# Optimization experiments

Hardware: AMD Instinct MI355X
Metric: run time of the kernel (lower is better)

Reference implementation:

```python
import jax, jax.numpy as jnp
import numpy as np

E, R, CIN, COUT = 8, 8, 256, 256
B, H, W = 16, 64, 64
DN = ('NCHW', 'OIHW', 'NCHW')


def setup_inputs() -> dict:
    key = jax.random.key(0)
    k1, k2, k3, k4 = jax.random.split(key, 4)
    x = jax.random.normal(k1, (B, CIN, H, W), jnp.float32)
    probs = jax.nn.softmax(jax.random.normal(k2, (E,), jnp.float32))
    # in conv: rank filters over in_channels, kernel (1,3); out conv: kernel (3,1)
    weight_in = jax.random.normal(k3, (E, R, CIN, 1, 3), jnp.float32) * 0.02
    weight_out = jax.random.normal(k4, (E, COUT, R, 3, 1), jnp.float32) * 0.02
    return {"x": x, "probs": probs, "weight_in": weight_in, "weight_out": weight_out}


def _expert_conv(x, w_in, w_out):
    # in conv: stride (1,1), padding (0,1) -> [B,R,H,W]
    h = jax.lax.conv_general_dilated(x, w_in, window_strides=(1, 1),
                                     padding=[(0, 0), (1, 1)], dimension_numbers=DN)
    # out conv: stride (1,1), padding (1,0) -> [B,COUT,H,W]
    return jax.lax.conv_general_dilated(h, w_out, window_strides=(1, 1),
                                        padding=[(1, 1), (0, 0)], dimension_numbers=DN)


def reference(x, probs, weight_in, weight_out):
    # vmap over experts replaces the Python loop; outs: [E,B,COUT,H,W]
    outs = jax.vmap(lambda wi, wo: _expert_conv(x, wi, wo))(weight_in, weight_out)
    # probability-weighted sum over experts (stack + sum in the original)
    return jnp.einsum('e,ebchw->bchw', probs, outs)
```

## Files before the change

kernel.cpp:

```cpp
#include <hip/hip_runtime.h>
#include <hip/hip_bf16.h>


typedef __bf16 bf16x8 __attribute__((ext_vector_type(8)));
typedef __bf16 bf16x4 __attribute__((ext_vector_type(4)));
typedef float  f32x4  __attribute__((ext_vector_type(4)));

#define CIN_  256
#define COUT_ 256
#define M1    64
#define K1    768
#define K2    192
#define CS    264
#define HS2   264

static __device__ __forceinline__ unsigned short f2bf(float f) {
    union { float f; unsigned u; } v; v.f = f;
    unsigned r = v.u + 0x7FFFu + ((v.u >> 16) & 1u);
    return (unsigned short)(r >> 16);
}

__global__ void prep_weights(const float* __restrict__ probs,
                             const float* __restrict__ w_in,
                             const float* __restrict__ w_out,
                             unsigned short* __restrict__ W1,
                             unsigned short* __restrict__ W2) {
    int idx = blockIdx.x * blockDim.x + threadIdx.x;
    if (idx < M1 * K1) {
        int er = idx / K1, rem = idx % K1;
        int kx = rem / CIN_, c = rem % CIN_;
        int e = er >> 3;
        W1[idx] = f2bf(probs[e] * w_in[(er * CIN_ + c) * 3 + kx]);
    } else {
        int i2 = idx - M1 * K1;
        int o = i2 / K2, rem = i2 % K2;
        int ky = rem / M1, er = rem % M1;
        int e = er >> 3, r = er & 7;
        W2[i2] = f2bf(w_out[((e * COUT_ + o) * 8 + r) * 3 + ky]);
    }
}

__global__ __launch_bounds__(256, 2)
void fused_kernel(const float* __restrict__ x,
                  const unsigned short* __restrict__ W1,
                  const unsigned short* __restrict__ W2,
                  float* __restrict__ out) {
    __shared__ unsigned short xs[66 * CS];
    __shared__ unsigned short hs[64 * HS2];
    const int bid  = blockIdx.x;
    const int b    = bid >> 5;
    const int y0   = (bid & 31) << 1;
    const int tid  = threadIdx.x;
    const int lane = tid & 63;
    const int wave = tid >> 6;
    const int g    = lane >> 4;
    const int lr   = lane & 15;

    bf16x8 w1f[3][8];
    {
        const unsigned short* w1p = W1 + (wave * 16 + lr) * K1 + g * 8;
        #pragma unroll
        for (int kx = 0; kx < 3; ++kx)
            #pragma unroll
            for (int cc = 0; cc < 8; ++cc)
                w1f[kx][cc] = *(const bf16x8*)(w1p + kx * CIN_ + cc * 32);
    }

    if (tid < 66) {
        int row = (tid < 33) ? 0 : 65;
        int col = (tid - (tid < 33 ? 0 : 33)) * 8;
        bf16x4 z4 = {};
        *(bf16x4*)&xs[row * CS + col] = z4;
        *(bf16x4*)&xs[row * CS + col + 4] = z4;
    }

    const int crow = tid >> 4;
    const int n4   = (tid & 15) << 2;
    const int swzt = (tid & 7) << 3;

    for (int yy = 0; yy < 4; ++yy) {
        const int y = y0 - 1 + yy;
        const bool yok = ((unsigned)y < 64u);
        __syncthreads();
        const float* xbase = x + ((b * CIN_ + crow) * 64 + (yok ? y : 0)) * 64 + n4;
        unsigned short* wr = &xs[(n4 + 1) * CS];
        #pragma unroll
        for (int r = 0; r < 4; ++r) {
            float4 ld[4];
            if (yok) {
                #pragma unroll
                for (int q = 0; q < 4; ++q)
                    ld[q] = *(const float4*)(xbase + (r * 4 + q) * 16 * 4096);
            } else {
                #pragma unroll
                for (int q = 0; q < 4; ++q) ld[q] = make_float4(0.f, 0.f, 0.f, 0.f);
            }
            #pragma unroll
            for (int q = 0; q < 4; ++q) {
                int cx = ((r * 4 + q) * 16 + crow) ^ swzt;
                wr[0 * CS + cx] = f2bf(ld[q].x);
                wr[1 * CS + cx] = f2bf(ld[q].y);
                wr[2 * CS + cx] = f2bf(ld[q].z);
                wr[3 * CS + cx] = f2bf(ld[q].w);
            }
        }
        __syncthreads();

        f32x4 acc[4];
        #pragma unroll
        for (int i = 0; i < 4; ++i) acc[i] = (f32x4){0.f, 0.f, 0.f, 0.f};
        #pragma unroll
        for (int kx = 0; kx < 3; ++kx) {
            int ns0 = lr + kx;
            int sz0 = (((ns0 - 1) >> 2) & 7) << 3;
            int ns1 = ns0 + 16, sz1 = (((ns1 - 1) >> 2) & 7) << 3;
            int ns2 = ns0 + 32, sz2 = (((ns2 - 1) >> 2) & 7) << 3;
            int ns3 = ns0 + 48, sz3 = (((ns3 - 1) >> 2) & 7) << 3;
            const unsigned short* r0  = &xs[ns0 * CS];
            const unsigned short* r1  = &xs[ns1 * CS];
            const unsigned short* r2p = &xs[ns2 * CS];
            const unsigned short* r3  = &xs[ns3 * CS];
            #pragma unroll
            for (int cc = 0; cc < 8; ++cc) {
                int co = cc * 32 + g * 8;
                acc[0] = __builtin_amdgcn_mfma_f32_16x16x32_bf16(
                    w1f[kx][cc], *(const bf16x8*)&r0[co ^ sz0], acc[0], 0, 0, 0);
                acc[1] = __builtin_amdgcn_mfma_f32_16x16x32_bf16(
                    w1f[kx][cc], *(const bf16x8*)&r1[co ^ sz1], acc[1], 0, 0, 0);
                acc[2] = __builtin_amdgcn_mfma_f32_16x16x32_bf16(
                    w1f[kx][cc], *(const bf16x8*)&r2p[co ^ sz2], acc[2], 0, 0, 0);
                acc[3] = __builtin_amdgcn_mfma_f32_16x16x32_bf16(
                    w1f[kx][cc], *(const bf16x8*)&r3[co ^ sz3], acc[3], 0, 0, 0);
            }
        }
        #pragma unroll
        for (int nt = 0; nt < 4; ++nt) {
            int n = nt * 16 + lr;
            bf16x4 pk;
            #pragma unroll
            for (int r2 = 0; r2 < 4; ++r2) pk[r2] = (__bf16)acc[nt][r2];
            int col = (yy * 64 + wave * 16 + g * 4) ^ ((n & 7) << 3);
            *(bf16x4*)&hs[n * HS2 + col] = pk;
        }
    }
    __syncthreads();

    bf16x8 w2f[4][6];
    #pragma unroll
    for (int ot = 0; ot < 4; ++ot)
        #pragma unroll
        for (int kc = 0; kc < 6; ++kc)
            w2f[ot][kc] = *(const bf16x8*)(W2 + ((wave * 4 + ot) * 16 + lr) * K2 +
                                           kc * 32 + g * 8);

    #pragma unroll
    for (int ry = 0; ry < 2; ++ry) {
        f32x4 acc2[4][4];
        #pragma unroll
        for (int ot = 0; ot < 4; ++ot)
            #pragma unroll
            for (int nt = 0; nt < 4; ++nt) acc2[ot][nt] = (f32x4){0.f, 0.f, 0.f, 0.f};

        #pragma unroll
        for (int kc = 0; kc < 6; ++kc) {
            bf16x8 bfrag[4];
            #pragma unroll
            for (int nt = 0; nt < 4; ++nt) {
                int n = nt * 16 + lr;
                int col = (ry * 64 + kc * 32 + g * 8) ^ ((n & 7) << 3);
                bfrag[nt] = *(const bf16x8*)&hs[n * HS2 + col];
            }
            #pragma unroll
            for (int ot = 0; ot < 4; ++ot)
                #pragma unroll
                for (int nt = 0; nt < 4; ++nt)
                    acc2[ot][nt] = __builtin_amdgcn_mfma_f32_16x16x32_bf16(
                        w2f[ot][kc], bfrag[nt], acc2[ot][nt], 0, 0, 0);
        }

        const int yo = y0 + ry;
        #pragma unroll
        for (int ot = 0; ot < 4; ++ot) {
            #pragma unroll
            for (int r2 = 0; r2 < 4; ++r2) {
                int o = (wave * 4 + ot) * 16 + g * 4 + r2;
                float* orow = out + ((b * COUT_ + o) * 64 + yo) * 64;
                #pragma unroll
                for (int nt = 0; nt < 4; ++nt)
                    orow[nt * 16 + lr] = acc2[ot][nt][r2];
            }
        }
    }
}

extern "C" void kernel_launch(void* const* d_in, const int* in_sizes, int n_in,
                              void* d_out, int out_size, void* d_ws, size_t ws_size,
                              hipStream_t stream) {
    const float* x     = (const float*)d_in[0];
    const float* probs = (const float*)d_in[1];
    const float* w_in  = (const float*)d_in[2];
    const float* w_out = (const float*)d_in[3];
    float* out = (float*)d_out;

    unsigned short* W1 = (unsigned short*)d_ws;
    unsigned short* W2 = W1 + M1 * K1;

    prep_weights<<<384, 256, 0, stream>>>(probs, w_in, w_out, W1, W2);
    fused_kernel<<<16 * 32, 256, 0, stream>>>(x, W1, W2, out);
}
```

Before: 49.25 us.

## Prefetch next input row into registers and pack bf16x4 LDS stores with new swizzle

```diff
diff --git a/kernel.cpp b/kernel.cpp
--- a/kernel.cpp
+++ b/kernel.cpp
@@ -11,13 +11,17 @@
 #define M1    64
 #define K1    768
 #define K2    192
-#define CS    264
-#define HS2   264
+#define CS    256
+#define HS    256
 
 static __device__ __forceinline__ unsigned short f2bf(float f) {
     union { float f; unsigned u; } v; v.f = f;
     unsigned r = v.u + 0x7FFFu + ((v.u >> 16) & 1u);
     return (unsigned short)(r >> 16);
+}
+
+static __device__ __forceinline__ int qsw(int r) {
+    return ((r ^ (r >> 3)) & 7) << 3;
 }
 
 __global__ void prep_weights(const float* __restrict__ probs,
@@ -46,7 +50,7 @@
                   const unsigned short* __restrict__ W2,
                   float* __restrict__ out) {
     __shared__ unsigned short xs[66 * CS];
-    __shared__ unsigned short hs[64 * HS2];
+    __shared__ unsigned short hs[64 * HS];
     const int bid  = blockIdx.x;
     const int b    = bid >> 5;
     const int y0   = (bid & 31) << 1;
@@ -66,92 +70,110 @@
                 w1f[kx][cc] = *(const bf16x8*)(w1p + kx * CIN_ + cc * 32);
     }
 
-    if (tid < 66) {
-        int row = (tid < 33) ? 0 : 65;
-        int col = (tid - (tid < 33 ? 0 : 33)) * 8;
-        bf16x4 z4 = {};
-        *(bf16x4*)&xs[row * CS + col] = z4;
-        *(bf16x4*)&xs[row * CS + col + 4] = z4;
-    }
-
-    const int crow = tid >> 4;
-    const int n4   = (tid & 15) << 2;
-    const int swzt = (tid & 7) << 3;
-
+    if (tid < 64) {
+        int row = (tid < 32) ? 0 : 65;
+        int col = (tid & 31) * 8;
+        bf16x8 z = {};
+        *(bf16x8*)&xs[row * CS + col] = z;
+    }
+
+    const int c0b = (tid >> 4) << 2;
+    const int n4  = (tid & 15) << 2;
+
+    f32x4 ld[4][4];
+
+    {
+        const int y = y0 - 1;
+        if (y >= 0) {
+            const float* xb = x + ((b * CIN_ + c0b) * 64 + y) * 64 + n4;
+            #pragma unroll
+            for (int it = 0; it < 4; ++it)
+                #pragma unroll
+                for (int i = 0; i < 4; ++i)
+                    ld[it][i] = *(const f32x4*)(xb + (it * 64 + i) * 4096);
+        } else {
+            #pragma unroll
+            for (int it = 0; it < 4; ++it)
+                #pragma unroll
+                for (int i = 0; i < 4; ++i)
+                    ld[it][i] = (f32x4){0.f, 0.f, 0.f, 0.f};
+        }
+    }
+
+    bf16x8 w2f[4][6];
+
+    #pragma unroll
     for (int yy = 0; yy < 4; ++yy) {
-        const int y = y0 - 1 + yy;
-        const bool yok = ((unsigned)y < 64u);
         __syncthreads();
-        const float* xbase = x + ((b * CIN_ + crow) * 64 + (yok ? y : 0)) * 64 + n4;
-        unsigned short* wr = &xs[(n4 + 1) * CS];
-        #pragma unroll
-        for (int r = 0; r < 4; ++r) {
-            float4 ld[4];
-            if (yok) {
-                #pragma unroll
-                for (int q = 0; q < 4; ++q)
-                    ld[q] = *(const float4*)(xbase + (r * 4 + q) * 16 * 4096);
+        #pragma unroll
+        for (int it = 0; it < 4; ++it) {
+            #pragma unroll
+            for (int j = 0; j < 4; ++j) {
+                int row = n4 + 1 + j;
+                int col = (it * 64 + c0b) ^ qsw(n4 + j);
+                bf16x4 pk;
+                #pragma unroll
+                for (int i = 0; i < 4; ++i) pk[i] = (__bf16)ld[it][i][j];
+                *(bf16x4*)&xs[row * CS + col] = pk;
+            }
+        }
+        __syncthreads();
+
+        if (yy < 3) {
+            const int y = y0 + yy;
+            if (y < 64) {
+                const float* xb = x + ((b * CIN_ + c0b) * 64 + y) * 64 + n4;
+                #pragma unroll
+                for (int it = 0; it < 4; ++it)
+                    #pragma unroll
+                    for (int i = 0; i < 4; ++i)
+                        ld[it][i] = *(const f32x4*)(xb + (it * 64 + i) * 4096);
             } else {
                 #pragma unroll
-                for (int q = 0; q < 4; ++q) ld[q] = make_float4(0.f, 0.f, 0.f, 0.f);
-            }
-            #pragma unroll
-            for (int q = 0; q < 4; ++q) {
-                int cx = ((r * 4 + q) * 16 + crow) ^ swzt;
-                wr[0 * CS + cx] = f2bf(ld[q].x);
-                wr[1 * CS + cx] = f2bf(ld[q].y);
-                wr[2 * CS + cx] = f2bf(ld[q].z);
-                wr[3 * CS + cx] = f2bf(ld[q].w);
-            }
-        }
-        __syncthreads();
+                for (int it = 0; it < 4; ++it)
+                    #pragma unroll
+                    for (int i = 0; i < 4; ++i)
+                        ld[it][i] = (f32x4){0.f, 0.f, 0.f, 0.f};
+            }
+        } else {
+            #pragma unroll
+            for (int ot = 0; ot < 4; ++ot)
+                #pragma unroll
+                for (int kc = 0; kc < 6; ++kc)
+                    w2f[ot][kc] = *(const bf16x8*)(W2 +
+                        ((wave * 4 + ot) * 16 + lr) * K2 + kc * 32 + g * 8);
+        }
 
         f32x4 acc[4];
         #pragma unroll
         for (int i = 0; i < 4; ++i) acc[i] = (f32x4){0.f, 0.f, 0.f, 0.f};
+
         #pragma unroll
         for (int kx = 0; kx < 3; ++kx) {
-            int ns0 = lr + kx;
-            int sz0 = (((ns0 - 1) >> 2) & 7) << 3;
-            int ns1 = ns0 + 16, sz1 = (((ns1 - 1) >> 2) & 7) << 3;
-            int ns2 = ns0 + 32, sz2 = (((ns2 - 1) >> 2) & 7) << 3;
-            int ns3 = ns0 + 48, sz3 = (((ns3 - 1) >> 2) & 7) << 3;
-            const unsigned short* r0  = &xs[ns0 * CS];
-            const unsigned short* r1  = &xs[ns1 * CS];
-            const unsigned short* r2p = &xs[ns2 * CS];
-            const unsigned short* r3  = &xs[ns3 * CS];
             #pragma unroll
             for (int cc = 0; cc < 8; ++cc) {
-                int co = cc * 32 + g * 8;
-                acc[0] = __builtin_amdgcn_mfma_f32_16x16x32_bf16(
-                    w1f[kx][cc], *(const bf16x8*)&r0[co ^ sz0], acc[0], 0, 0, 0);
-                acc[1] = __builtin_amdgcn_mfma_f32_16x16x32_bf16(
-                    w1f[kx][cc], *(const bf16x8*)&r1[co ^ sz1], acc[1], 0, 0, 0);
-                acc[2] = __builtin_amdgcn_mfma_f32_16x16x32_bf16(
-                    w1f[kx][cc], *(const bf16x8*)&r2p[co ^ sz2], acc[2], 0, 0, 0);
-                acc[3] = __builtin_amdgcn_mfma_f32_16x16x32_bf16(
-                    w1f[kx][cc], *(const bf16x8*)&r3[co ^ sz3], acc[3], 0, 0, 0);
-            }
-        }
+                #pragma unroll
+                for (int nt = 0; nt < 4; ++nt) {
+                    int r = nt * 16 + lr + kx - 1;
+                    bf16x8 bfv = *(const bf16x8*)&xs[(r + 1) * CS +
+                                                     ((cc * 32 + g * 8) ^ qsw(r))];
+                    acc[nt] = __builtin_amdgcn_mfma_f32_16x16x32_bf16(
+                        w1f[kx][cc], bfv, acc[nt], 0, 0, 0);
+                }
+            }
+        }
+
         #pragma unroll
         for (int nt = 0; nt < 4; ++nt) {
             int n = nt * 16 + lr;
+            int col = (yy * 64 + wave * 16 + g * 4) ^ qsw(n);
             bf16x4 pk;
             #pragma unroll
             for (int r2 = 0; r2 < 4; ++r2) pk[r2] = (__bf16)acc[nt][r2];
-            int col = (yy * 64 + wave * 16 + g * 4) ^ ((n & 7) << 3);
-            *(bf16x4*)&hs[n * HS2 + col] = pk;
+            *(bf16x4*)&hs[n * HS + col] = pk;
         }
     }
     __syncthreads();
-
-    bf16x8 w2f[4][6];
-    #pragma unroll
-    for (int ot = 0; ot < 4; ++ot)
-        #pragma unroll
-        for (int kc = 0; kc < 6; ++kc)
-            w2f[ot][kc] = *(const bf16x8*)(W2 + ((wave * 4 + ot) * 16 + lr) * K2 +
-                                           kc * 32 + g * 8);
 
     #pragma unroll
     for (int ry = 0; ry < 2; ++ry) {
@@ -167,8 +189,8 @@
             #pragma unroll
             for (int nt = 0; nt < 4; ++nt) {
                 int n = nt * 16 + lr;
-                int col = (ry * 64 + kc * 32 + g * 8) ^ ((n & 7) << 3);
-                bfrag[nt] = *(const bf16x8*)&hs[n * HS2 + col];
+                bfrag[nt] = *(const bf16x8*)&hs[n * HS +
+                    ((ry * 64 + kc * 32 + g * 8) ^ qsw(n))];
             }
             #pragma unroll
             for (int ot = 0; ot < 4; ++ot)
```

Result: slower. 122.9 us (+149.7%).
